# Kernel optimization log

Measured on AMD Instinct MI355X. Metric: run time of the kernel, lower is better.

## Reference

```python
import jax, jax.numpy as jnp
import numpy as np

B, N = 16, 2048
NOTE, BEAT_H, MEAS_H, FINAL_H = 512, 128, 64, 128
NUM_BEATS, NUM_MEAS = 256, 64
OUT = 11            # output_size; QPM_INDEX = 0
QPM = 0


def _uniform(k, shape, fan):
    b = 1.0 / np.sqrt(fan)
    return jax.random.uniform(k, shape, jnp.float32, -b, b)


def _lstm_cell(x, h, c, wih, whh, bih, bhh):
    g = x @ wih.T + bih + h @ whh.T + bhh
    ii, ff, gg, oo = jnp.split(g, 4, axis=-1)
    c2 = jax.nn.sigmoid(ff) * c + jax.nn.sigmoid(ii) * jnp.tanh(gg)
    return jax.nn.sigmoid(oo) * jnp.tanh(c2), c2


def setup_inputs() -> dict:
    key = jax.random.key(0)
    ks = jax.random.split(key, 20)
    note_emb = jax.random.normal(ks[0], (B, N, NOTE), jnp.float32)
    beat_emb = jax.random.normal(ks[1], (B, NUM_BEATS, BEAT_H), jnp.float32)
    measure_emb = jax.random.normal(ks[2], (B, NUM_MEAS, MEAS_H), jnp.float32)
    beat_numbers = jnp.sort(jax.random.randint(ks[3], (B, N), 0, NUM_BEATS), axis=1)
    measure_numbers = beat_numbers // (NUM_BEATS // NUM_MEAS)
    tin = BEAT_H + MEAS_H + 1 + (OUT - 1)   # beat-tempo LSTM input size
    fin = NOTE + BEAT_H + MEAS_H + OUT      # final LSTM input size
    d = OUT - 1
    return {
        "note_emb": note_emb, "beat_emb": beat_emb, "measure_emb": measure_emb,
        "beat_numbers": beat_numbers, "measure_numbers": measure_numbers,
        "Wa": _uniform(ks[4], (d, d), d), "ba": _uniform(ks[5], (d,), d),
        "ctx": _uniform(ks[6], (d,), d),
        "Wih_t": _uniform(ks[7], (4 * BEAT_H, tin), BEAT_H),
        "Whh_t": _uniform(ks[8], (4 * BEAT_H, BEAT_H), BEAT_H),
        "bih_t": _uniform(ks[9], (4 * BEAT_H,), BEAT_H),
        "bhh_t": _uniform(ks[10], (4 * BEAT_H,), BEAT_H),
        "Wih_f": _uniform(ks[11], (4 * FINAL_H, fin), FINAL_H),
        "Whh_f": _uniform(ks[12], (4 * FINAL_H, FINAL_H), FINAL_H),
        "bih_f": _uniform(ks[13], (4 * FINAL_H,), FINAL_H),
        "bhh_f": _uniform(ks[14], (4 * FINAL_H,), FINAL_H),
        "W_fc": _uniform(ks[15], (d, FINAL_H), FINAL_H),
        "b_fc": _uniform(ks[16], (d,), FINAL_H),
        "W_tfc": _uniform(ks[17], (1, BEAT_H), BEAT_H),
        "b_tfc": _uniform(ks[18], (1,), BEAT_H),
    }


def _decode(note_emb, beat_emb, measure_emb, beat_numbers, measure_numbers,
            Wa, ba, ctx, Wih_t, Whh_t, bih_t, bhh_t,
            Wih_f, Whh_f, bih_f, bhh_f, W_fc, b_fc, W_tfc, b_tfc):
    Bn, Nn = note_emb.shape[0], note_emb.shape[1]
    d = W_fc.shape[0]  # OUT - 1
    zs_beat = jnp.maximum(beat_numbers - beat_numbers[:, :1], 0)
    zs_meas = jnp.maximum(measure_numbers - measure_numbers[:, :1], 0)
    diff = jnp.diff(beat_numbers, axis=1)
    # beat_changed: first step forced to 1, then diff of beat numbers
    changed_all = jnp.concatenate([jnp.ones((Bn, 1), diff.dtype), diff], axis=1) > 0
    pos = jnp.arange(Nn)
    bidx = jnp.arange(Bn)

    carry0 = (
        jnp.zeros((Bn, BEAT_H)), jnp.zeros((Bn, BEAT_H)),        # tempo h, c
        jnp.zeros((Bn, FINAL_H)), jnp.zeros((Bn, FINAL_H)),      # final h, c
        jnp.zeros((Bn, d + 1)),                                   # prev_out
        jnp.zeros((Bn, beat_emb.shape[1], d)),                    # beat_results
        jnp.zeros((Bn, Nn, d + 1)),                               # out_total
    )

    def step(carry, i):
        th, tc, fh, fc_, prev_out, beat_results, out_total = carry
        changed = changed_all[:, i]                                # [B] bool
        # --- get_beat_corresp_out: notes j < i in the beat just finished ---
        prev_beat = beat_numbers[:, jnp.maximum(i - 1, 0)]         # [B]
        note_mask = (beat_numbers == prev_beat[:, None]) & (pos[None, :] < i)
        x = out_total[:, :, QPM + 1:]                              # [B,N,d]
        sim = (x @ Wa.T + ba) @ ctx                                # [B,N]
        sim = jnp.where(note_mask, sim, -1e9)
        w = jax.nn.softmax(sim, axis=1)
        result_node = jnp.einsum('bn,bnd->bd', w, x)
        result_node = jnp.where(note_mask.any(axis=1)[:, None], result_node, 0.0)
        cb = zs_beat[:, i]
        cm = zs_meas[:, i]
        # scatter result_node into beat_results only for batches whose beat changed
        old = beat_results[bidx, cb]
        beat_results = beat_results.at[bidx, cb].set(
            jnp.where(changed[:, None], result_node, old))
        # --- beat tempo RNN step (only applied where changed) ---
        tempo_in = jnp.concatenate([
            beat_emb[bidx, cb], measure_emb[bidx, cm],
            prev_out[:, QPM:QPM + 1], beat_results[bidx, cb]], axis=-1)
        th2, tc2 = _lstm_cell(tempo_in, th, tc, Wih_t, Whh_t, bih_t, bhh_t)
        th = jnp.where(changed[:, None], th2, th)
        tc = jnp.where(changed[:, None], tc2, tc)
        tmp_tempo = th2 @ W_tfc.T + b_tfc                          # [B,1]
        prev_out = prev_out.at[:, QPM:QPM + 1].set(
            jnp.where(changed[:, None], tmp_tempo, prev_out[:, QPM:QPM + 1]))
        # --- final note-level LSTM step (all batches) ---
        fin_in = jnp.concatenate([
            note_emb[:, i], beat_emb[bidx, cb], measure_emb[bidx, cm], prev_out], axis=-1)
        fh, fc_ = _lstm_cell(fin_in, fh, fc_, Wih_f, Whh_f, bih_f, bhh_f)
        out = fh @ W_fc.T + b_fc                                   # [B,d]
        prev_out = jnp.concatenate([prev_out[:, :QPM + 1], out], axis=-1)
        out_total = out_total.at[:, i].set(prev_out)
        return (th, tc, fh, fc_, prev_out, beat_results, out_total), None

    carry, _ = jax.lax.scan(step, carry0, jnp.arange(Nn))
    out_total = carry[-1]
    # zero out padded notes (note embedding all-zero rows)
    pad = (note_emb.sum(-1) == 0)[:, :, None]
    return jnp.where(pad, 0.0, out_total)


def reference(note_emb, beat_emb, measure_emb, beat_numbers, measure_numbers,
              Wa, ba, ctx, Wih_t, Whh_t, bih_t, bhh_t,
              Wih_f, Whh_f, bih_f, bhh_f, W_fc, b_fc, W_tfc, b_tfc):
    return _decode(note_emb, beat_emb, measure_emb, beat_numbers, measure_numbers,
                   Wa, ba, ctx, Wih_t, Whh_t, bih_t, bhh_t,
                   Wih_f, Whh_f, bih_f, bhh_f, W_fc, b_fc, W_tfc, b_tfc)
```

## Files before the change

### kernel.cpp

```cpp
#include <hip/hip_runtime.h>
#include <cstdint>
#include <cstddef>

#define B_      16
#define N_      2048
#define NOTE_   512
#define BEAT_H_ 128
#define MEAS_H_ 64
#define NBEATS_ 256
#define NMEAS_  64
#define OUT_    11
#define D_      10
#define TSTRIDE 136

typedef float f32x4 __attribute__((ext_vector_type(4)));
typedef unsigned int u32x4 __attribute__((ext_vector_type(4)));
typedef _Float16 h2v __attribute__((ext_vector_type(2)));

__device__ __forceinline__ float fexp2_(float x) {
#if __has_builtin(__builtin_amdgcn_exp2f)
    return __builtin_amdgcn_exp2f(x);
#else
    return exp2f(x);
#endif
}
__device__ __forceinline__ float frcp_(float x) {
#if __has_builtin(__builtin_amdgcn_rcpf)
    return __builtin_amdgcn_rcpf(x);
#else
    return 1.0f / x;
#endif
}
__device__ __forceinline__ float sigm_(float x) {
    return frcp_(1.0f + fexp2_(-1.4426950408889634f * x));
}
__device__ __forceinline__ float tanh_(float x) {
    return 1.0f - 2.0f * frcp_(fexp2_(2.8853900817779268f * x) + 1.0f);
}

__device__ __forceinline__ void bar_lds_() {
    asm volatile("s_waitcnt lgkmcnt(0)\n\ts_barrier" ::: "memory");
}

#define DOT4(va, vb) ((va).x * (vb).x + (va).y * (vb).y + (va).z * (vb).z + (va).w * (vb).w)

__device__ __forceinline__ float dot2f_(unsigned wu, unsigned hu, float c) {
    union { unsigned u; h2v h; } a, bb;
    a.u = wu; bb.u = hu;
#if __has_builtin(__builtin_amdgcn_fdot2)
    return __builtin_amdgcn_fdot2(a.h, bb.h, c, false);
#else
    return c + (float)a.h[0] * (float)bb.h[0] + (float)a.h[1] * (float)bb.h[1];
#endif
}

__device__ __align__(16) _Float16 g_whh_h16[512 * 128];
__device__ float g_bias_eff[512];
__device__ float g_wtail0[512];
__device__ __align__(16) _Float16 g_wht_h16[512 * TSTRIDE];

__global__ __launch_bounds__(256) void pad_k(const float* __restrict__ note,
                                             int* __restrict__ padf) {
    int wave = threadIdx.x >> 6, lane = threadIdx.x & 63;
    int r = blockIdx.x * 4 + wave;
    const float* row = note + ((size_t)r << 9);
    float s = 0.f;
#pragma unroll
    for (int u = 0; u < 8; ++u) s += row[lane + (u << 6)];
#pragma unroll
    for (int off = 32; off; off >>= 1) s += __shfl_xor(s, off, 64);
    if (lane == 0) padf[r] = (s == 0.0f) ? 1 : 0;
}

__global__ __launch_bounds__(128) void fold_whh(
    const float* __restrict__ Whh_f, const float* __restrict__ Wih_f,
    const float* __restrict__ W_fc, const float* __restrict__ b_fc) {
    int gr = blockIdx.x;
    int t = threadIdx.x;
    __shared__ float tail[OUT_];
    if (t < OUT_) tail[t] = Wih_f[(size_t)gr * 715 + 704 + t];
    __syncthreads();
    float m = Whh_f[(size_t)gr * 128 + t];
#pragma unroll
    for (int d = 0; d < D_; ++d) m += tail[1 + d] * W_fc[d * 128 + t];
    g_whh_h16[(size_t)gr * 128 + t] = (_Float16)m;
    if (t == 0) {
        float bb = 0.f;
#pragma unroll
        for (int d = 0; d < D_; ++d) bb += tail[1 + d] * b_fc[d];
        g_bias_eff[gr] = bb;
        g_wtail0[gr] = tail[0];
    }
}

__global__ __launch_bounds__(128) void fold_wht(const float* __restrict__ Whh_t) {
    int gr = blockIdx.x, t = threadIdx.x;
    g_wht_h16[(size_t)gr * TSTRIDE + t] = (_Float16)Whh_t[(size_t)gr * 128 + t];
    if (t < TSTRIDE - 128) g_wht_h16[(size_t)gr * TSTRIDE + 128 + t] = (_Float16)0.f;
}

__global__ __launch_bounds__(256) void tempo_pre_k(
    const float* __restrict__ beat, const float* __restrict__ meas,
    const int* __restrict__ bnum, const int* __restrict__ mnum,
    const float* __restrict__ Wih_t, const float* __restrict__ bih_t,
    const float* __restrict__ bhh_t, float* __restrict__ tpre) {
    __shared__ float sin_[16][192];
    int b = blockIdx.x, qt = blockIdx.y;
    int t = threadIdx.x;
    int bn0 = bnum[b << 11], mn0 = mnum[b << 11];
    for (int idx = t; idx < 16 * 192; idx += 256) {
        int qq = idx / 192, kk = idx - qq * 192;
        int q = qt * 16 + qq;
        float v;
        if (kk < 128) {
            v = beat[(size_t)(b * NBEATS_ + q) * 128 + kk];
        } else {
            int cm = ((q + bn0) >> 2) - mn0;
            if (cm > 63) cm = 63;
            if (cm < 0) cm = 0;
            v = meas[(size_t)(b * NMEAS_ + cm) * 64 + (kk - 128)];
        }
        sin_[qq][kk] = v;
    }
    __syncthreads();
    for (int half = 0; half < 2; ++half) {
        int j = t + half * 256;
        const float* wr = Wih_t + (size_t)j * 203;
        float bias = bih_t[j] + bhh_t[j];
        float acc[16] = {};
        for (int k = 0; k < 192; ++k) {
            float w = wr[k];
#pragma unroll
            for (int qq = 0; qq < 16; ++qq) acc[qq] += w * sin_[qq][k];
        }
        for (int qq = 0; qq < 16; ++qq)
            tpre[(size_t)(b * NBEATS_ + qt * 16 + qq) * 512 + j] = acc[qq] + bias;
    }
}

__global__ __launch_bounds__(256) void fin_pre_gemm(
    const float* __restrict__ note, const float* __restrict__ beat,
    const float* __restrict__ meas, const int* __restrict__ bnum,
    const int* __restrict__ mnum, const float* __restrict__ Wih_f,
    const float* __restrict__ bih_f, const float* __restrict__ bhh_f,
    float* __restrict__ finp) {
    __shared__ float As[16][64];
    __shared__ float Bs[16][64];
    int t = threadIdx.x;
    int r0 = blockIdx.x * 64;
    int j0 = blockIdx.y * 64;

    int am = t >> 2, alane = t & 3;
    int r = r0 + am;
    int b = r >> 11;
    int rb = b << 11;
    int cb = bnum[r] - bnum[rb];
    int cm = mnum[r] - mnum[rb];
    const float* arow_note = note + ((size_t)r << 9);
    const float* arow_beat = beat + ((size_t)(b * NBEATS_ + cb) << 7);
    const float* arow_meas = meas + ((size_t)(b * NMEAS_ + cm) << 6);

    int jj = t >> 2, blane = t & 3;
    const float* brow = Wih_f + (size_t)(j0 + jj) * 715;

    int tm0 = (t & 15) * 4, tn0 = (t >> 4) * 4;
    float acc[4][4] = {};

    for (int k0 = 0; k0 < 704; k0 += 16) {
        int ka = k0 + alane * 4;
        float4 av;
        if (ka < 512)      av = *(const float4*)(arow_note + ka);
        else if (ka < 640) av = *(const float4*)(arow_beat + (ka - 512));
        else               av = *(const float4*)(arow_meas + (ka - 640));
        int kb = k0 + blane * 4;
        float b0 = brow[kb], b1 = brow[kb + 1], b2 = brow[kb + 2], b3 = brow[kb + 3];
        __syncthreads();
        As[alane * 4 + 0][am] = av.x;
        As[alane * 4 + 1][am] = av.y;
        As[alane * 4 + 2][am] = av.z;
        As[alane * 4 + 3][am] = av.w;
        Bs[blane * 4 + 0][jj] = b0;
        Bs[blane * 4 + 1][jj] = b1;
        Bs[blane * 4 + 2][jj] = b2;
        Bs[blane * 4 + 3][jj] = b3;
        __syncthreads();
#pragma unroll
        for (int kk = 0; kk < 16; ++kk) {
            float4 a4 = *(const float4*)&As[kk][tm0];
            float4 b4 = *(const float4*)&Bs[kk][tn0];
            float aa[4] = {a4.x, a4.y, a4.z, a4.w};
            float bb[4] = {b4.x, b4.y, b4.z, b4.w};
#pragma unroll
            for (int mi = 0; mi < 4; ++mi)
#pragma unroll
                for (int ni = 0; ni < 4; ++ni) acc[mi][ni] += aa[mi] * bb[ni];
        }
    }
    float bias[4], beff[4];
#pragma unroll
    for (int ni = 0; ni < 4; ++ni) {
        int j = j0 + tn0 + ni;
        bias[ni] = bih_f[j] + bhh_f[j];
        beff[ni] = g_bias_eff[j];
    }
#pragma unroll
    for (int mi = 0; mi < 4; ++mi) {
        int rr = r0 + tm0 + mi;
        float eb = (rr & 2047) ? 1.0f : 0.0f;
        float4 o;
        o.x = acc[mi][0] + bias[0] + eb * beff[0];
        o.y = acc[mi][1] + bias[1] + eb * beff[1];
        o.z = acc[mi][2] + bias[2] + eb * beff[2];
        o.w = acc[mi][3] + bias[3] + eb * beff[3];
        *(float4*)(finp + ((size_t)rr << 9) + j0 + tn0) = o;
    }
}

__global__ __launch_bounds__(512)
__attribute__((amdgpu_waves_per_eu(2, 2)))
void decode_seq(
    const float* __restrict__ finp, const float* __restrict__ tpre,
    const int* __restrict__ bnum, const int* __restrict__ padf,
    const float* __restrict__ Wih_t,
    const float* __restrict__ W_fc, const float* __restrict__ b_fc,
    const float* __restrict__ W_tfc, const float* __restrict__ b_tfc,
    const float* __restrict__ Wa, const float* __restrict__ ba,
    const float* __restrict__ ctx, float* __restrict__ out,
    float* __restrict__ xg) {
    __shared__ __align__(16) _Float16 wht16_s[512 * TSTRIDE];
    __shared__ __align__(16) _Float16 ht16_s[128];
    __shared__ __align__(16) _Float16 hf16_s[128];
    __shared__ __align__(16) float hf_s[128];
    __shared__ float cf_s[128];
    __shared__ float ht_s[128];
    __shared__ float ct_s[128];
    __shared__ __align__(16) float g_s[512];
    __shared__ float gt_s[512];
    __shared__ float wtail0_s[512];
    __shared__ float wfcT[128][12];
    __shared__ float wtfc_s[128];
    __shared__ float bfc_s[12];
    __shared__ float cur_res[12];
    __shared__ float v_s[12];
    __shared__ float sc_s[4];
    __shared__ unsigned long long padw_s[32];
    __shared__ unsigned short run_start_s[300];
    __shared__ short run_cb_s[300];
    __shared__ int nruns_s;

    int t = threadIdx.x, lane = t & 63, wave = t >> 6;
    int b = blockIdx.x;

    u32x4 wf0, wf1, wf2, wf3, wf4, wf5, wf6, wf7;
    u32x4 wf8, wf9, wf10, wf11, wf12, wf13, wf14, wf15;
    {
        const u32x4* wfp = (const u32x4*)(g_whh_h16 + (size_t)t * 128);
        wf0 = wfp[0];   wf1 = wfp[1];   wf2 = wfp[2];   wf3 = wfp[3];
        wf4 = wfp[4];   wf5 = wfp[5];   wf6 = wfp[6];   wf7 = wfp[7];
        wf8 = wfp[8];   wf9 = wfp[9];   wf10 = wfp[10]; wf11 = wfp[11];
        wf12 = wfp[12]; wf13 = wfp[13]; wf14 = wfp[14]; wf15 = wfp[15];
    }
    asm volatile("" : "+v"(wf0), "+v"(wf1), "+v"(wf2), "+v"(wf3),
                      "+v"(wf4), "+v"(wf5), "+v"(wf6), "+v"(wf7));
    asm volatile("" : "+v"(wf8), "+v"(wf9), "+v"(wf10), "+v"(wf11),
                      "+v"(wf12), "+v"(wf13), "+v"(wf14), "+v"(wf15));

    float wtail0_r = g_wtail0[t];
    wtail0_s[t] = wtail0_r;
    float wiht_r[OUT_];
#pragma unroll
    for (int u = 0; u < OUT_; ++u) wiht_r[u] = Wih_t[(size_t)t * 203 + 192 + u];

    {
        const uint4* src = (const uint4*)g_wht_h16;
        uint4* dst = (uint4*)wht16_s;
#pragma unroll
        for (int k = 0; k < 17; ++k) dst[t + 512 * k] = src[t + 512 * k];
    }
    for (int k = t; k < 128 * D_; k += 512) {
        int d = k >> 7, r = k & 127;
        wfcT[r][d] = W_fc[k];
    }
    if (t < 128) {
        wtfc_s[t] = W_tfc[t];
        hf_s[t] = 0.f; cf_s[t] = 0.f; ht_s[t] = 0.f; ct_s[t] = 0.f;
        ht16_s[t] = (_Float16)0.f;
        hf16_s[t] = (_Float16)0.f;
    }
    if (t < D_) {
        bfc_s[t] = b_fc[t];
        cur_res[t] = 0.f;
        float vv = 0.f;
        for (int m = 0; m < D_; ++m) vv += ctx[m] * Wa[m * D_ + t];
        v_s[t] = vv;
    }
    if (t == 10) {
        float cc = 0.f;
        for (int m = 0; m < D_; ++m) cc += ba[m] * ctx[m];
        sc_s[0] = cc;
        sc_s[1] = b_tfc[0];
        sc_s[2] = 0.f;
    }
    if (wave >= 2 && wave < 6) {
        for (int jj = 0; jj < 8; ++jj) {
            int j = (wave - 2) * 8 + jj;
            int pv = padf[(b << 11) + j * 64 + lane];
            unsigned long long m = __ballot(pv != 0);
            if (lane == 0) padw_s[j] = m;
        }
    }
    const int* bnb = bnum + (b << 11);
    int bn0 = bnb[0];
    int base = t * 4;
    int bvm = (base == 0) ? 0 : bnb[base - 1];
    int bv0 = bnb[base], bv1 = bnb[base + 1], bv2 = bnb[base + 2], bv3 = bnb[base + 3];
    if (base == 0) bvm = bv0 - 1;
    int c = (bv0 != bvm) + (bv1 != bv0) + (bv2 != bv1) + (bv3 != bv2);
    ((int*)g_s)[t] = c;
    __syncthreads();
    if (wave == 0) {
        int c8[8], s = 0;
#pragma unroll
        for (int j = 0; j < 8; ++j) { c8[j] = ((int*)g_s)[lane * 8 + j]; s += c8[j]; }
        int incl = s;
#pragma unroll
        for (int off = 1; off < 64; off <<= 1) {
            int n = __shfl_up(incl, off, 64);
            if (lane >= off) incl += n;
        }
        int run = incl - s;
#pragma unroll
        for (int j = 0; j < 8; ++j) { ((int*)gt_s)[lane * 8 + j] = run; run += c8[j]; }
        if (lane == 63) nruns_s = incl;
    }
    __syncthreads();
    {
        int O = ((int*)gt_s)[t];
        if (bv0 != bvm) { run_start_s[O] = (unsigned short)(base + 0); run_cb_s[O] = (short)(bv0 - bn0); O++; }
        if (bv1 != bv0) { run_start_s[O] = (unsigned short)(base + 1); run_cb_s[O] = (short)(bv1 - bn0); O++; }
        if (bv2 != bv1) { run_start_s[O] = (unsigned short)(base + 2); run_cb_s[O] = (short)(bv2 - bn0); O++; }
        if (bv3 != bv2) { run_start_s[O] = (unsigned short)(base + 3); run_cb_s[O] = (short)(bv3 - bn0); O++; }
    }
    __syncthreads();
    int nruns_r = nruns_s;

    const float* finrow = finp + ((size_t)b << 11) * 512;
    float* xgb = xg + ((size_t)(b << 11)) * 16;
    float gf_cur = finrow[t];
    float gf_n1 = finrow[512 + t];
    float gt_pre = tpre[(size_t)(b * NBEATS_) * 512 + t];
    int cur_run = -1, next_start = 0, run_s = 0, S_prev = 0;

    for (int i = 0; i < N_; ++i) {
        bool changed = (i == next_start);
        if (changed) {
            cur_run++;
            S_prev = run_s;
            run_s = i;
            next_start = (cur_run + 1 < nruns_r) ? (int)run_start_s[cur_run + 1] : 4096;
        }
        float gf_n2 = finrow[(size_t)(i + 2) * 512 + t];
        float prev0 = sc_s[2];

        float acc;
        {
            const u32x4* hq = (const u32x4*)hf16_s;
            float a0 = 0.f, a1 = 0.f, a2 = 0.f, a3 = 0.f;
#define MSTEP(W, K)                                            \
            { u32x4 H = hq[K];                                 \
              a0 = dot2f_(W.x, H.x, a0);                       \
              a1 = dot2f_(W.y, H.y, a1);                       \
              a2 = dot2f_(W.z, H.z, a2);                       \
              a3 = dot2f_(W.w, H.w, a3); }
            MSTEP(wf0, 0)   MSTEP(wf1, 1)   MSTEP(wf2, 2)   MSTEP(wf3, 3)
            MSTEP(wf4, 4)   MSTEP(wf5, 5)   MSTEP(wf6, 6)   MSTEP(wf7, 7)
            MSTEP(wf8, 8)   MSTEP(wf9, 9)   MSTEP(wf10, 10) MSTEP(wf11, 11)
            MSTEP(wf12, 12) MSTEP(wf13, 13) MSTEP(wf14, 14) MSTEP(wf15, 15)
#undef MSTEP
            acc = (a0 + a1) + (a2 + a3);
        }
        {
            float g = gf_cur + acc;
            if (!changed) g += wtail0_r * prev0;
            g_s[t] = g;
        }
        gf_cur = gf_n1;
        gf_n1 = gf_n2;

        if (wave == 1 && i > 0) {
            int dd = lane >> 3, rl = lane & 7;
            int d2i = 8 + dd;
            float po1 = 0.f, po2 = 0.f;
            for (int k2 = 0; k2 < 16; ++k2) {
                int r = rl + (k2 << 3);
                float hv = hf_s[r];
                po1 += hv * wfcT[r][dd];
                if (d2i < D_) po2 += hv * wfcT[r][d2i];
            }
            po1 += __shfl_xor(po1, 1); po1 += __shfl_xor(po1, 2); po1 += __shfl_xor(po1, 4);
            po2 += __shfl_xor(po2, 1); po2 += __shfl_xor(po2, 2); po2 += __shfl_xor(po2, 4);
            int pi = i - 1;
            int pd = (int)((padw_s[pi >> 6] >> (pi & 63)) & 1ULL);
            float* orow = out + (size_t)((b << 11) + pi) * OUT_;
            float* xrow = xgb + (size_t)pi * 16;
            if (rl == 0) {
                float od = po1 + bfc_s[dd];
                xrow[dd] = od;
                orow[1 + dd] = pd ? 0.f : od;
                if (d2i < D_) {
                    float od2 = po2 + bfc_s[d2i];
                    xrow[d2i] = od2;
                    orow[1 + d2i] = pd ? 0.f : od2;
                }
            }
            if (lane == 1) orow[0] = pd ? 0.f : prev0;
        }

        if (changed) {
            float acct;
            {
                const u32x4* wq = (const u32x4*)(wht16_s + (size_t)t * TSTRIDE);
                const u32x4* hq = (const u32x4*)ht16_s;
                float a0 = 0.f, a1 = 0.f, a2 = 0.f, a3 = 0.f;
#pragma unroll
                for (int k = 0; k < 16; ++k) {
                    u32x4 W = wq[k];
                    u32x4 H = hq[k];
                    a0 = dot2f_(W.x, H.x, a0);
                    a1 = dot2f_(W.y, H.y, a1);
                    a2 = dot2f_(W.z, H.z, a2);
                    a3 = dot2f_(W.w, H.w, a3);
                }
                acct = (a0 + a1) + (a2 + a3);
            }
            gt_s[t] = gt_pre + acct + wiht_r[0] * prev0;
            __syncthreads();
        } else {
            bar_lds_();
        }

        if (!changed) {
            if (wave < 2) {
                int rr = lane + (wave << 6);
                float gi = g_s[rr], gff = g_s[128 + rr], gg = g_s[256 + rr], go = g_s[384 + rr];
                float c2 = sigm_(gff) * cf_s[rr] + sigm_(gi) * tanh_(gg);
                float h2 = sigm_(go) * tanh_(c2);
                cf_s[rr] = c2;
                hf_s[rr] = h2;
                hf16_s[rr] = (_Float16)h2;
            }
        } else {
            if (wave == 0) {
                int L = i - S_prev;
                const float4* xb = (const float4*)(xgb + (size_t)S_prev * 16);
                float lmax = -1e30f;
                for (int tt = lane; tt < L; tt += 64) {
                    float4 q0 = xb[tt * 4 + 0], q1 = xb[tt * 4 + 1], q2 = xb[tt * 4 + 2];
                    float s = sc_s[0] + q0.x * v_s[0] + q0.y * v_s[1] + q0.z * v_s[2] +
                              q0.w * v_s[3] + q1.x * v_s[4] + q1.y * v_s[5] +
                              q1.z * v_s[6] + q1.w * v_s[7] + q2.x * v_s[8] + q2.y * v_s[9];
                    lmax = fmaxf(lmax, s);
                }
#pragma unroll
                for (int off = 32; off; off >>= 1)
                    lmax = fmaxf(lmax, __shfl_xor(lmax, off, 64));
                float lsum = 0.f, lacc[D_] = {};
                for (int tt = lane; tt < L; tt += 64) {
                    float4 q0 = xb[tt * 4 + 0], q1 = xb[tt * 4 + 1], q2 = xb[tt * 4 + 2];
                    float s = sc_s[0] + q0.x * v_s[0] + q0.y * v_s[1] + q0.z * v_s[2] +
                              q0.w * v_s[3] + q1.x * v_s[4] + q1.y * v_s[5] +
                              q1.z * v_s[6] + q1.w * v_s[7] + q2.x * v_s[8] + q2.y * v_s[9];
                    float w = fexp2_(1.4426950408889634f * (s - lmax));
                    lsum += w;
                    lacc[0] += w * q0.x; lacc[1] += w * q0.y; lacc[2] += w * q0.z;
                    lacc[3] += w * q0.w; lacc[4] += w * q1.x; lacc[5] += w * q1.y;
                    lacc[6] += w * q1.z; lacc[7] += w * q1.w; lacc[8] += w * q2.x;
                    lacc[9] += w * q2.y;
                }
#pragma unroll
                for (int off = 32; off; off >>= 1) {
                    lsum += __shfl_xor(lsum, off, 64);
#pragma unroll
                    for (int d = 0; d < D_; ++d) lacc[d] += __shfl_xor(lacc[d], off, 64);
                }
                if (lane == 0) {
                    if (L > 0) {
                        float inv = 1.0f / lsum;
#pragma unroll
                        for (int d = 0; d < D_; ++d) cur_res[d] = lacc[d] * inv;
                    } else {
#pragma unroll
                        for (int d = 0; d < D_; ++d) cur_res[d] = 0.f;
                    }
                }
            }
            bar_lds_();
            {
                float gv = gt_s[t];
#pragma unroll
                for (int d = 0; d < D_; ++d) gv += wiht_r[1 + d] * cur_res[d];
                gt_s[t] = gv;
            }
            bar_lds_();
            if (wave == 0) {
                float p = 0.f;
#pragma unroll
                for (int hb = 0; hb < 2; ++hb) {
                    int rr = lane + (hb << 6);
                    float gi = gt_s[rr], gff = gt_s[128 + rr], gg = gt_s[256 + rr],
                          go = gt_s[384 + rr];
                    float c2 = sigm_(gff) * ct_s[rr] + sigm_(gi) * tanh_(gg);
                    float h2 = sigm_(go) * tanh_(c2);
                    ct_s[rr] = c2;
                    ht_s[rr] = h2;
                    ht16_s[rr] = (_Float16)h2;
                    p += h2 * wtfc_s[rr];
                }
#pragma unroll
                for (int off = 32; off; off >>= 1) p += __shfl_xor(p, off, 64);
                float tnew = p + sc_s[1];
                if (lane == 0) sc_s[2] = tnew;
#pragma unroll
                for (int hb = 0; hb < 2; ++hb) {
                    int rr = lane + (hb << 6);
                    float gi = g_s[rr] + wtail0_s[rr] * tnew;
                    float gff = g_s[128 + rr] + wtail0_s[128 + rr] * tnew;
                    float gg = g_s[256 + rr] + wtail0_s[256 + rr] * tnew;
                    float go = g_s[384 + rr] + wtail0_s[384 + rr] * tnew;
                    float c2 = sigm_(gff) * cf_s[rr] + sigm_(gi) * tanh_(gg);
                    float h2 = sigm_(go) * tanh_(c2);
                    cf_s[rr] = c2;
                    hf_s[rr] = h2;
                    hf16_s[rr] = (_Float16)h2;
                }
            }
            if (cur_run + 1 < nruns_r)
                gt_pre = tpre[(size_t)(b * NBEATS_ + (int)run_cb_s[cur_run + 1]) * 512 + t];
        }
        bar_lds_();
    }

    if (wave == 1) {
        int dd = lane >> 3, rl = lane & 7;
        int d2i = 8 + dd;
        float po1 = 0.f, po2 = 0.f;
        for (int k2 = 0; k2 < 16; ++k2) {
            int r = rl + (k2 << 3);
            float hv = hf_s[r];
            po1 += hv * wfcT[r][dd];
            if (d2i < D_) po2 += hv * wfcT[r][d2i];
        }
        po1 += __shfl_xor(po1, 1); po1 += __shfl_xor(po1, 2); po1 += __shfl_xor(po1, 4);
        po2 += __shfl_xor(po2, 1); po2 += __shfl_xor(po2, 2); po2 += __shfl_xor(po2, 4);
        int pi = N_ - 1;
        int pd = (int)((padw_s[pi >> 6] >> (pi & 63)) & 1ULL);
        float* orow = out + (size_t)((b << 11) + pi) * OUT_;
        if (rl == 0) {
            orow[1 + dd] = pd ? 0.f : (po1 + bfc_s[dd]);
            if (d2i < D_) orow[1 + d2i] = pd ? 0.f : (po2 + bfc_s[d2i]);
        }
        if (lane == 1) orow[0] = pd ? 0.f : sc_s[2];
    }
}

extern "C" void kernel_launch(void* const* d_in, const int* in_sizes, int n_in,
                              void* d_out, int out_size, void* d_ws, size_t ws_size,
                              hipStream_t stream) {
    const float* note  = (const float*)d_in[0];
    const float* beat  = (const float*)d_in[1];
    const float* meas  = (const float*)d_in[2];
    const int*   bnum  = (const int*)d_in[3];
    const int*   mnum  = (const int*)d_in[4];
    const float* Wa    = (const float*)d_in[5];
    const float* ba    = (const float*)d_in[6];
    const float* ctx   = (const float*)d_in[7];
    const float* Wih_t = (const float*)d_in[8];
    const float* Whh_t = (const float*)d_in[9];
    const float* bih_t = (const float*)d_in[10];
    const float* bhh_t = (const float*)d_in[11];
    const float* Wih_f = (const float*)d_in[12];
    const float* Whh_f = (const float*)d_in[13];
    const float* bih_f = (const float*)d_in[14];
    const float* bhh_f = (const float*)d_in[15];
    const float* W_fc  = (const float*)d_in[16];
    const float* b_fc  = (const float*)d_in[17];
    const float* W_tfc = (const float*)d_in[18];
    const float* b_tfc = (const float*)d_in[19];
    float* out = (float*)d_out;

    char* ws = (char*)d_ws;
    float* finp = (float*)ws;
    float* tpre = (float*)(ws + (size_t)64 * 1024 * 1024);
    int*   padf = (int*)(ws + (size_t)72 * 1024 * 1024);
    float* xg   = (float*)(ws + (size_t)73 * 1024 * 1024);

    pad_k<<<8192, 256, 0, stream>>>(note, padf);
    fold_whh<<<512, 128, 0, stream>>>(Whh_f, Wih_f, W_fc, b_fc);
    fold_wht<<<512, 128, 0, stream>>>(Whh_t);
    tempo_pre_k<<<dim3(16, 16), 256, 0, stream>>>(beat, meas, bnum, mnum, Wih_t,
                                                  bih_t, bhh_t, tpre);
    fin_pre_gemm<<<dim3(512, 8), 256, 0, stream>>>(note, beat, meas, bnum, mnum,
                                                   Wih_f, bih_f, bhh_f, finp);
    decode_seq<<<16, 512, 0, stream>>>(finp, tpre, bnum, padf, Wih_t,
                                       W_fc, b_fc, W_tfc, b_tfc, Wa, ba, ctx,
                                       out, xg);
}
```

Before: 4.239 ms.

## Restructure decode loop so each thread computes all four gates for one hidden unit

The sequential decode kernel moves from 512 threads, one gate row each, to 384 threads. The 256 gate threads each hold four gate rows split over two K-halves, combine the halves with a cross-lane shuffle, and apply the LSTM cell in registers. This removes the g_s/gt_s LDS round trip and one barrier per step on the non-beat-change path. Double-buffered h vectors let the next step's reads proceed without a separate sync, and dedicated waves handle the output projection and attention. The cost is more register pressure (128 weight VGPRs per thread) and reloading the Wih_t tail from global memory on every beat change.

```diff
diff --git a/kernel.cpp b/kernel.cpp
--- a/kernel.cpp
+++ b/kernel.cpp
@@ -42,8 +42,6 @@
     asm volatile("s_waitcnt lgkmcnt(0)\n\ts_barrier" ::: "memory");
 }
 
-#define DOT4(va, vb) ((va).x * (vb).x + (va).y * (vb).y + (va).z * (vb).z + (va).w * (vb).w)
-
 __device__ __forceinline__ float dot2f_(unsigned wu, unsigned hu, float c) {
     union { unsigned u; h2v h; } a, bb;
     a.u = wu; bb.u = hu;
@@ -53,6 +51,11 @@
     return c + (float)a.h[0] * (float)bb.h[0] + (float)a.h[1] * (float)bb.h[1];
 #endif
 }
+#define DQ(W, H, S)                                                           \
+    do {                                                                      \
+        S = dot2f_((W).x, (H).x, S); S = dot2f_((W).y, (H).y, S);             \
+        S = dot2f_((W).z, (H).z, S); S = dot2f_((W).w, (H).w, S);             \
+    } while (0)
 
 __device__ __align__(16) _Float16 g_whh_h16[512 * 128];
 __device__ float g_bias_eff[512];
@@ -216,7 +219,7 @@
     }
 }
 
-__global__ __launch_bounds__(512)
+__global__ __launch_bounds__(384)
 __attribute__((amdgpu_waves_per_eu(2, 2)))
 void decode_seq(
     const float* __restrict__ finp, const float* __restrict__ tpre,
@@ -228,64 +231,113 @@
     const float* __restrict__ ctx, float* __restrict__ out,
     float* __restrict__ xg) {
     __shared__ __align__(16) _Float16 wht16_s[512 * TSTRIDE];
-    __shared__ __align__(16) _Float16 ht16_s[128];
-    __shared__ __align__(16) _Float16 hf16_s[128];
-    __shared__ __align__(16) float hf_s[128];
-    __shared__ float cf_s[128];
-    __shared__ float ht_s[128];
-    __shared__ float ct_s[128];
-    __shared__ __align__(16) float g_s[512];
-    __shared__ float gt_s[512];
-    __shared__ float wtail0_s[512];
+    __shared__ __align__(16) _Float16 hf16_s[2][128];
+    __shared__ __align__(16) _Float16 ht16_s[2][128];
+    __shared__ __align__(16) float hf_s[2][128];
     __shared__ float wfcT[128][12];
     __shared__ float wtfc_s[128];
     __shared__ float bfc_s[12];
     __shared__ float cur_res[12];
     __shared__ float v_s[12];
     __shared__ float sc_s[4];
+    __shared__ float tred_s[4];
     __shared__ unsigned long long padw_s[32];
     __shared__ unsigned short run_start_s[300];
     __shared__ short run_cb_s[300];
     __shared__ int nruns_s;
 
-    int t = threadIdx.x, lane = t & 63, wave = t >> 6;
+    int t = threadIdx.x, gl = t & 63, gw = t >> 6;
     int b = blockIdx.x;
-
-    u32x4 wf0, wf1, wf2, wf3, wf4, wf5, wf6, wf7;
-    u32x4 wf8, wf9, wf10, wf11, wf12, wf13, wf14, wf15;
+    bool is_gate = gw < 4;
+    int row = (gw << 5) + (gl & 31);
+    int kh = gl >> 5;
+    if (!is_gate) row = 0;
+
+    int* counts = (int*)&wfcT[0][0];
+    int* offs = counts + 512;
+    const int* bnb = bnum + (b << 11);
+    int bn0 = bnb[0];
+    for (int c = t; c < 512; c += 384) {
+        int base = c * 4;
+        int bvm = (base == 0) ? (bnb[0] - 1) : bnb[base - 1];
+        int v0 = bnb[base], v1 = bnb[base + 1], v2 = bnb[base + 2], v3 = bnb[base + 3];
+        counts[c] = (v0 != bvm) + (v1 != v0) + (v2 != v1) + (v3 != v2);
+    }
+    __syncthreads();
+    if (gw == 0) {
+        int c8[8], s = 0;
+#pragma unroll
+        for (int j = 0; j < 8; ++j) { c8[j] = counts[gl * 8 + j]; s += c8[j]; }
+        int incl = s;
+#pragma unroll
+        for (int off = 1; off < 64; off <<= 1) {
+            int n = __shfl_up(incl, off, 64);
+            if (gl >= off) incl += n;
+        }
+        int run = incl - s;
+#pragma unroll
+        for (int j = 0; j < 8; ++j) { offs[gl * 8 + j] = run; run += c8[j]; }
+        if (gl == 63) nruns_s = incl;
+    }
+    __syncthreads();
+    for (int c = t; c < 512; c += 384) {
+        int base = c * 4;
+        int bvm = (base == 0) ? (bnb[0] - 1) : bnb[base - 1];
+        int v0 = bnb[base], v1 = bnb[base + 1], v2 = bnb[base + 2], v3 = bnb[base + 3];
+        int O = offs[c];
+        if (v0 != bvm) { run_start_s[O] = (unsigned short)(base + 0); run_cb_s[O] = (short)(v0 - bn0); O++; }
+        if (v1 != v0) { run_start_s[O] = (unsigned short)(base + 1); run_cb_s[O] = (short)(v1 - bn0); O++; }
+        if (v2 != v1) { run_start_s[O] = (unsigned short)(base + 2); run_cb_s[O] = (short)(v2 - bn0); O++; }
+        if (v3 != v2) { run_start_s[O] = (unsigned short)(base + 3); run_cb_s[O] = (short)(v3 - bn0); O++; }
+    }
+    __syncthreads();
+    int nruns_r = nruns_s;
+
+    u32x4 A0, A1, A2, A3, A4, A5, A6, A7;
+    u32x4 Bw0, Bw1, Bw2, Bw3, Bw4, Bw5, Bw6, Bw7;
+    u32x4 C0, C1, C2, C3, C4, C5, C6, C7;
+    u32x4 Dw0, Dw1, Dw2, Dw3, Dw4, Dw5, Dw6, Dw7;
     {
-        const u32x4* wfp = (const u32x4*)(g_whh_h16 + (size_t)t * 128);
-        wf0 = wfp[0];   wf1 = wfp[1];   wf2 = wfp[2];   wf3 = wfp[3];
-        wf4 = wfp[4];   wf5 = wfp[5];   wf6 = wfp[6];   wf7 = wfp[7];
-        wf8 = wfp[8];   wf9 = wfp[9];   wf10 = wfp[10]; wf11 = wfp[11];
-        wf12 = wfp[12]; wf13 = wfp[13]; wf14 = wfp[14]; wf15 = wfp[15];
-    }
-    asm volatile("" : "+v"(wf0), "+v"(wf1), "+v"(wf2), "+v"(wf3),
-                      "+v"(wf4), "+v"(wf5), "+v"(wf6), "+v"(wf7));
-    asm volatile("" : "+v"(wf8), "+v"(wf9), "+v"(wf10), "+v"(wf11),
-                      "+v"(wf12), "+v"(wf13), "+v"(wf14), "+v"(wf15));
-
-    float wtail0_r = g_wtail0[t];
-    wtail0_s[t] = wtail0_r;
-    float wiht_r[OUT_];
-#pragma unroll
-    for (int u = 0; u < OUT_; ++u) wiht_r[u] = Wih_t[(size_t)t * 203 + 192 + u];
+        int rr = is_gate ? row : 0;
+        const u32x4* pa = (const u32x4*)(g_whh_h16 + ((size_t)(rr) << 7) + (kh << 6));
+        const u32x4* pb = (const u32x4*)(g_whh_h16 + ((size_t)(rr + 128) << 7) + (kh << 6));
+        const u32x4* pc = (const u32x4*)(g_whh_h16 + ((size_t)(rr + 256) << 7) + (kh << 6));
+        const u32x4* pd = (const u32x4*)(g_whh_h16 + ((size_t)(rr + 384) << 7) + (kh << 6));
+        A0 = pa[0]; A1 = pa[1]; A2 = pa[2]; A3 = pa[3];
+        A4 = pa[4]; A5 = pa[5]; A6 = pa[6]; A7 = pa[7];
+        Bw0 = pb[0]; Bw1 = pb[1]; Bw2 = pb[2]; Bw3 = pb[3];
+        Bw4 = pb[4]; Bw5 = pb[5]; Bw6 = pb[6]; Bw7 = pb[7];
+        C0 = pc[0]; C1 = pc[1]; C2 = pc[2]; C3 = pc[3];
+        C4 = pc[4]; C5 = pc[5]; C6 = pc[6]; C7 = pc[7];
+        Dw0 = pd[0]; Dw1 = pd[1]; Dw2 = pd[2]; Dw3 = pd[3];
+        Dw4 = pd[4]; Dw5 = pd[5]; Dw6 = pd[6]; Dw7 = pd[7];
+    }
+    asm volatile("" : "+v"(A0), "+v"(A1), "+v"(A2), "+v"(A3),
+                      "+v"(A4), "+v"(A5), "+v"(A6), "+v"(A7));
+    asm volatile("" : "+v"(Bw0), "+v"(Bw1), "+v"(Bw2), "+v"(Bw3),
+                      "+v"(Bw4), "+v"(Bw5), "+v"(Bw6), "+v"(Bw7));
+    asm volatile("" : "+v"(C0), "+v"(C1), "+v"(C2), "+v"(C3),
+                      "+v"(C4), "+v"(C5), "+v"(C6), "+v"(C7));
+    asm volatile("" : "+v"(Dw0), "+v"(Dw1), "+v"(Dw2), "+v"(Dw3),
+                      "+v"(Dw4), "+v"(Dw5), "+v"(Dw6), "+v"(Dw7));
+
+    float wt0a = g_wtail0[row], wt0b = g_wtail0[row + 128],
+          wt0c = g_wtail0[row + 256], wt0d = g_wtail0[row + 384];
 
     {
         const uint4* src = (const uint4*)g_wht_h16;
         uint4* dst = (uint4*)wht16_s;
-#pragma unroll
-        for (int k = 0; k < 17; ++k) dst[t + 512 * k] = src[t + 512 * k];
-    }
-    for (int k = t; k < 128 * D_; k += 512) {
+        for (int k = t; k < 512 * TSTRIDE / 8; k += 384) dst[k] = src[k];
+    }
+    for (int k = t; k < 128 * D_; k += 384) {
         int d = k >> 7, r = k & 127;
         wfcT[r][d] = W_fc[k];
     }
     if (t < 128) {
         wtfc_s[t] = W_tfc[t];
-        hf_s[t] = 0.f; cf_s[t] = 0.f; ht_s[t] = 0.f; ct_s[t] = 0.f;
-        ht16_s[t] = (_Float16)0.f;
-        hf16_s[t] = (_Float16)0.f;
+        hf16_s[0][t] = (_Float16)0.f; hf16_s[1][t] = (_Float16)0.f;
+        ht16_s[0][t] = (_Float16)0.f; ht16_s[1][t] = (_Float16)0.f;
+        hf_s[0][t] = 0.f; hf_s[1][t] = 0.f;
     }
     if (t < D_) {
         bfc_s[t] = b_fc[t];
@@ -301,54 +353,31 @@
         sc_s[1] = b_tfc[0];
         sc_s[2] = 0.f;
     }
-    if (wave >= 2 && wave < 6) {
+    if (is_gate) {
         for (int jj = 0; jj < 8; ++jj) {
-            int j = (wave - 2) * 8 + jj;
-            int pv = padf[(b << 11) + j * 64 + lane];
+            int j = gw * 8 + jj;
+            int pv = padf[(b << 11) + j * 64 + gl];
             unsigned long long m = __ballot(pv != 0);
-            if (lane == 0) padw_s[j] = m;
-        }
-    }
-    const int* bnb = bnum + (b << 11);
-    int bn0 = bnb[0];
-    int base = t * 4;
-    int bvm = (base == 0) ? 0 : bnb[base - 1];
-    int bv0 = bnb[base], bv1 = bnb[base + 1], bv2 = bnb[base + 2], bv3 = bnb[base + 3];
-    if (base == 0) bvm = bv0 - 1;
-    int c = (bv0 != bvm) + (bv1 != bv0) + (bv2 != bv1) + (bv3 != bv2);
-    ((int*)g_s)[t] = c;
+            if (gl == 0) padw_s[j] = m;
+        }
+    }
     __syncthreads();
-    if (wave == 0) {
-        int c8[8], s = 0;
-#pragma unroll
-        for (int j = 0; j < 8; ++j) { c8[j] = ((int*)g_s)[lane * 8 + j]; s += c8[j]; }
-        int incl = s;
-#pragma unroll
-        for (int off = 1; off < 64; off <<= 1) {
-            int n = __shfl_up(incl, off, 64);
-            if (lane >= off) incl += n;
-        }
-        int run = incl - s;
-#pragma unroll
-        for (int j = 0; j < 8; ++j) { ((int*)gt_s)[lane * 8 + j] = run; run += c8[j]; }
-        if (lane == 63) nruns_s = incl;
-    }
-    __syncthreads();
-    {
-        int O = ((int*)gt_s)[t];
-        if (bv0 != bvm) { run_start_s[O] = (unsigned short)(base + 0); run_cb_s[O] = (short)(bv0 - bn0); O++; }
-        if (bv1 != bv0) { run_start_s[O] = (unsigned short)(base + 1); run_cb_s[O] = (short)(bv1 - bn0); O++; }
-        if (bv2 != bv1) { run_start_s[O] = (unsigned short)(base + 2); run_cb_s[O] = (short)(bv2 - bn0); O++; }
-        if (bv3 != bv2) { run_start_s[O] = (unsigned short)(base + 3); run_cb_s[O] = (short)(bv3 - bn0); O++; }
-    }
-    __syncthreads();
-    int nruns_r = nruns_s;
 
     const float* finrow = finp + ((size_t)b << 11) * 512;
     float* xgb = xg + ((size_t)(b << 11)) * 16;
-    float gf_cur = finrow[t];
-    float gf_n1 = finrow[512 + t];
-    float gt_pre = tpre[(size_t)(b * NBEATS_) * 512 + t];
+    float fiA_c = 0, fiB_c = 0, fiC_c = 0, fiD_c = 0;
+    float fiA_1 = 0, fiB_1 = 0, fiC_1 = 0, fiD_1 = 0;
+    float gtA = 0, gtB = 0, gtC = 0, gtD = 0;
+    if (is_gate && kh == 0) {
+        fiA_c = finrow[row];       fiB_c = finrow[row + 128];
+        fiC_c = finrow[row + 256]; fiD_c = finrow[row + 384];
+        fiA_1 = finrow[512 + row];       fiB_1 = finrow[512 + row + 128];
+        fiC_1 = finrow[512 + row + 256]; fiD_1 = finrow[512 + row + 384];
+        const float* tp0 = tpre + (size_t)(b * NBEATS_) * 512;
+        gtA = tp0[row];       gtB = tp0[row + 128];
+        gtC = tp0[row + 256]; gtD = tp0[row + 384];
+    }
+    float cf_r = 0.f, ct_r = 0.f;
     int cur_run = -1, next_start = 0, run_s = 0, S_prev = 0;
 
     for (int i = 0; i < N_; ++i) {
@@ -359,41 +388,83 @@
             run_s = i;
             next_start = (cur_run + 1 < nruns_r) ? (int)run_start_s[cur_run + 1] : 4096;
         }
-        float gf_n2 = finrow[(size_t)(i + 2) * 512 + t];
+        int wb = i & 1, rb = wb ^ 1;
+        int rp = cur_run & 1;
         float prev0 = sc_s[2];
 
-        float acc;
-        {
-            const u32x4* hq = (const u32x4*)hf16_s;
-            float a0 = 0.f, a1 = 0.f, a2 = 0.f, a3 = 0.f;
-#define MSTEP(W, K)                                            \
-            { u32x4 H = hq[K];                                 \
-              a0 = dot2f_(W.x, H.x, a0);                       \
-              a1 = dot2f_(W.y, H.y, a1);                       \
-              a2 = dot2f_(W.z, H.z, a2);                       \
-              a3 = dot2f_(W.w, H.w, a3); }
-            MSTEP(wf0, 0)   MSTEP(wf1, 1)   MSTEP(wf2, 2)   MSTEP(wf3, 3)
-            MSTEP(wf4, 4)   MSTEP(wf5, 5)   MSTEP(wf6, 6)   MSTEP(wf7, 7)
-            MSTEP(wf8, 8)   MSTEP(wf9, 9)   MSTEP(wf10, 10) MSTEP(wf11, 11)
-            MSTEP(wf12, 12) MSTEP(wf13, 13) MSTEP(wf14, 14) MSTEP(wf15, 15)
-#undef MSTEP
-            acc = (a0 + a1) + (a2 + a3);
-        }
-        {
-            float g = gf_cur + acc;
-            if (!changed) g += wtail0_r * prev0;
-            g_s[t] = g;
-        }
-        gf_cur = gf_n1;
-        gf_n1 = gf_n2;
-
-        if (wave == 1 && i > 0) {
-            int dd = lane >> 3, rl = lane & 7;
+        float si = 0.f, sf = 0.f, sg = 0.f, so = 0.f;
+        float ti = 0.f, tf = 0.f, tg = 0.f, to_ = 0.f;
+        float wA[OUT_], wB[OUT_], wC[OUT_], wD[OUT_];
+        float fA2 = 0, fB2 = 0, fC2 = 0, fD2 = 0;
+
+        if (is_gate) {
+            if (kh == 0) {
+                const float* fnx = finrow + (size_t)(i + 2) * 512;
+                fA2 = fnx[row];       fB2 = fnx[row + 128];
+                fC2 = fnx[row + 256]; fD2 = fnx[row + 384];
+            }
+            {
+                const u32x4* hq = (const u32x4*)&hf16_s[rb][0] + (kh << 3);
+                u32x4 h0 = hq[0], h1 = hq[1], h2 = hq[2], h3 = hq[3];
+                u32x4 h4 = hq[4], h5 = hq[5], h6 = hq[6], h7 = hq[7];
+                DQ(A0, h0, si); DQ(A1, h1, si); DQ(A2, h2, si); DQ(A3, h3, si);
+                DQ(A4, h4, si); DQ(A5, h5, si); DQ(A6, h6, si); DQ(A7, h7, si);
+                DQ(Bw0, h0, sf); DQ(Bw1, h1, sf); DQ(Bw2, h2, sf); DQ(Bw3, h3, sf);
+                DQ(Bw4, h4, sf); DQ(Bw5, h5, sf); DQ(Bw6, h6, sf); DQ(Bw7, h7, sf);
+                DQ(C0, h0, sg); DQ(C1, h1, sg); DQ(C2, h2, sg); DQ(C3, h3, sg);
+                DQ(C4, h4, sg); DQ(C5, h5, sg); DQ(C6, h6, sg); DQ(C7, h7, sg);
+                DQ(Dw0, h0, so); DQ(Dw1, h1, so); DQ(Dw2, h2, so); DQ(Dw3, h3, so);
+                DQ(Dw4, h4, so); DQ(Dw5, h5, so); DQ(Dw6, h6, so); DQ(Dw7, h7, so);
+            }
+            if (kh == 0) {
+                si += fiA_c; sf += fiB_c; sg += fiC_c; so += fiD_c;
+                if (!changed) {
+                    si += wt0a * prev0; sf += wt0b * prev0;
+                    sg += wt0c * prev0; so += wt0d * prev0;
+                }
+            }
+            si += __shfl_xor(si, 32, 64);
+            sf += __shfl_xor(sf, 32, 64);
+            sg += __shfl_xor(sg, 32, 64);
+            so += __shfl_xor(so, 32, 64);
+            fiA_c = fiA_1; fiB_c = fiB_1; fiC_c = fiC_1; fiD_c = fiD_1;
+            fiA_1 = fA2; fiB_1 = fB2; fiC_1 = fC2; fiD_1 = fD2;
+
+            if (changed) {
+                if (kh == 0) {
+#pragma unroll
+                    for (int u = 0; u < OUT_; ++u) {
+                        wA[u] = Wih_t[(size_t)row * 203 + 192 + u];
+                        wB[u] = Wih_t[(size_t)(row + 128) * 203 + 192 + u];
+                        wC[u] = Wih_t[(size_t)(row + 256) * 203 + 192 + u];
+                        wD[u] = Wih_t[(size_t)(row + 384) * 203 + 192 + u];
+                    }
+                }
+                const u32x4* tq = (const u32x4*)&ht16_s[rp ^ 1][0] + (kh << 3);
+                u32x4 t0 = tq[0], t1 = tq[1], t2 = tq[2], t3 = tq[3];
+                u32x4 t4 = tq[4], t5 = tq[5], t6 = tq[6], t7 = tq[7];
+                const u32x4* qa = (const u32x4*)(wht16_s + (size_t)row * TSTRIDE + (kh << 6));
+                const u32x4* qb = (const u32x4*)(wht16_s + (size_t)(row + 128) * TSTRIDE + (kh << 6));
+                const u32x4* qc = (const u32x4*)(wht16_s + (size_t)(row + 256) * TSTRIDE + (kh << 6));
+                const u32x4* qd = (const u32x4*)(wht16_s + (size_t)(row + 384) * TSTRIDE + (kh << 6));
+#pragma unroll
+                for (int k = 0; k < 8; ++k) {
+                    u32x4 hh = (k == 0) ? t0 : (k == 1) ? t1 : (k == 2) ? t2 :
+                               (k == 3) ? t3 : (k == 4) ? t4 : (k == 5) ? t5 :
+                               (k == 6) ? t6 : t7;
+                    u32x4 va = qa[k], vb = qb[k], vc = qc[k], vd = qd[k];
+                    DQ(va, hh, ti); DQ(vb, hh, tf); DQ(vc, hh, tg); DQ(vd, hh, to_);
+                }
+            }
+        }
+
+        if (gw == 4 && i > 0) {
+            int dd = gl >> 3, rl = gl & 7;
             int d2i = 8 + dd;
             float po1 = 0.f, po2 = 0.f;
             for (int k2 = 0; k2 < 16; ++k2) {
                 int r = rl + (k2 << 3);
-                float hv = hf_s[r];
+                float hv = hf_s[rb][r];
                 po1 += hv * wfcT[r][dd];
                 if (d2i < D_) po2 += hv * wfcT[r][d2i];
             }
@@ -413,48 +484,26 @@
                     orow[1 + d2i] = pd ? 0.f : od2;
                 }
             }
-            if (lane == 1) orow[0] = pd ? 0.f : prev0;
-        }
-
-        if (changed) {
-            float acct;
-            {
-                const u32x4* wq = (const u32x4*)(wht16_s + (size_t)t * TSTRIDE);
-                const u32x4* hq = (const u32x4*)ht16_s;
-                float a0 = 0.f, a1 = 0.f, a2 = 0.f, a3 = 0.f;
-#pragma unroll
-                for (int k = 0; k < 16; ++k) {
-                    u32x4 W = wq[k];
-                    u32x4 H = hq[k];
-                    a0 = dot2f_(W.x, H.x, a0);
-                    a1 = dot2f_(W.y, H.y, a1);
-                    a2 = dot2f_(W.z, H.z, a2);
-                    a3 = dot2f_(W.w, H.w, a3);
-                }
-                acct = (a0 + a1) + (a2 + a3);
-            }
-            gt_s[t] = gt_pre + acct + wiht_r[0] * prev0;
+            if (gl == 1) orow[0] = pd ? 0.f : prev0;
+        }
+
+        if (!changed) {
+            if (is_gate) {
+                float c2 = sigm_(sf) * cf_r + sigm_(si) * tanh_(sg);
+                float h2 = sigm_(so) * tanh_(c2);
+                cf_r = c2;
+                if (kh == 0) {
+                    hf16_s[wb][row] = (_Float16)h2;
+                    hf_s[wb][row] = h2;
+                }
+            }
+        } else {
             __syncthreads();
-        } else {
-            bar_lds_();
-        }
-
-        if (!changed) {
-            if (wave < 2) {
-                int rr = lane + (wave << 6);
-                float gi = g_s[rr], gff = g_s[128 + rr], gg = g_s[256 + rr], go = g_s[384 + rr];
-                float c2 = sigm_(gff) * cf_s[rr] + sigm_(gi) * tanh_(gg);
-                float h2 = sigm_(go) * tanh_(c2);
-                cf_s[rr] = c2;
-                hf_s[rr] = h2;
-                hf16_s[rr] = (_Float16)h2;
-            }
-        } else {
-            if (wave == 0) {
+            if (gw == 5) {
                 int L = i - S_prev;
                 const float4* xb = (const float4*)(xgb + (size_t)S_prev * 16);
                 float lmax = -1e30f;
-                for (int tt = lane; tt < L; tt += 64) {
+                for (int tt = gl; tt < L; tt += 64) {
                     float4 q0 = xb[tt * 4 + 0], q1 = xb[tt * 4 + 1], q2 = xb[tt * 4 + 2];
                     float s = sc_s[0] + q0.x * v_s[0] + q0.y * v_s[1] + q0.z * v_s[2] +
                               q0.w * v_s[3] + q1.x * v_s[4] + q1.y * v_s[5] +
@@ -465,7 +514,7 @@
                 for (int off = 32; off; off >>= 1)
                     lmax = fmaxf(lmax, __shfl_xor(lmax, off, 64));
                 float lsum = 0.f, lacc[D_] = {};
-                for (int tt = lane; tt < L; tt += 64) {
+                for (int tt = gl; tt < L; tt += 64) {
                     float4 q0 = xb[tt * 4 + 0], q1 = xb[tt * 4 + 1], q2 = xb[tt * 4 + 2];
                     float s = sc_s[0] + q0.x * v_s[0] + q0.y * v_s[1] + q0.z * v_s[2] +
                               q0.w * v_s[3] + q1.x * v_s[4] + q1.y * v_s[5] +
@@ -483,7 +532,7 @@
 #pragma unroll
                     for (int d = 0; d < D_; ++d) lacc[d] += __shfl_xor(lacc[d], off, 64);
                 }
-                if (lane == 0) {
+                if (gl == 0) {
                     if (L > 0) {
                         float inv = 1.0f / lsum;
 #pragma unroll
@@ -495,58 +544,65 @@
                 }
             }
             bar_lds_();
+            if (is_gate) {
+                if (kh == 0) {
+                    float ta = gtA + wA[0] * prev0, tb = gtB + wB[0] * prev0;
+                    float tc = gtC + wC[0] * prev0, td = gtD + wD[0] * prev0;
+#pragma unroll
+                    for (int d = 0; d < D_; ++d) {
+                        float cr = cur_res[d];
+                        ta += wA[1 + d] * cr; tb += wB[1 + d] * cr;
+                        tc += wC[1 + d] * cr; td += wD[1 + d] * cr;
+                    }
+                    ti += ta; tf += tb; tg += tc; to_ += td;
+                }
+                ti += __shfl_xor(ti, 32, 64);
+                tf += __shfl_xor(tf, 32, 64);
+                tg += __shfl_xor(tg, 32, 64);
+                to_ += __shfl_xor(to_, 32, 64);
+                float tc2 = sigm_(tf) * ct_r + sigm_(ti) * tanh_(tg);
+                float th2 = sigm_(to_) * tanh_(tc2);
+                ct_r = tc2;
+                if (kh == 0) ht16_s[rp][row] = (_Float16)th2;
+                float p = (kh == 0) ? th2 * wtfc_s[row] : 0.f;
+#pragma unroll
+                for (int off = 32; off; off >>= 1) p += __shfl_xor(p, off, 64);
+                if (gl == 0) tred_s[gw] = p;
+            }
+            bar_lds_();
             {
-                float gv = gt_s[t];
-#pragma unroll
-                for (int d = 0; d < D_; ++d) gv += wiht_r[1 + d] * cur_res[d];
-                gt_s[t] = gv;
-            }
-            bar_lds_();
-            if (wave == 0) {
-                float p = 0.f;
-#pragma unroll
-                for (int hb = 0; hb < 2; ++hb) {
-                    int rr = lane + (hb << 6);
-                    float gi = gt_s[rr], gff = gt_s[128 + rr], gg = gt_s[256 + rr],
-                          go = gt_s[384 + rr];
-                    float c2 = sigm_(gff) * ct_s[rr] + sigm_(gi) * tanh_(gg);
-                    float h2 = sigm_(go) * tanh_(c2);
-                    ct_s[rr] = c2;
-                    ht_s[rr] = h2;
-                    ht16_s[rr] = (_Float16)h2;
-                    p += h2 * wtfc_s[rr];
-                }
-#pragma unroll
-                for (int off = 32; off; off >>= 1) p += __shfl_xor(p, off, 64);
-                float tnew = p + sc_s[1];
-                if (lane == 0) sc_s[2] = tnew;
-#pragma unroll
-                for (int hb = 0; hb < 2; ++hb) {
-                    int rr = lane + (hb << 6);
-                    float gi = g_s[rr] + wtail0_s[rr] * tnew;
-                    float gff = g_s[128 + rr] + wtail0_s[128 + rr] * tnew;
-                    float gg = g_s[256 + rr] + wtail0_s[256 + rr] * tnew;
-                    float go = g_s[384 + rr] + wtail0_s[384 + rr] * tnew;
-                    float c2 = sigm_(gff) * cf_s[rr] + sigm_(gi) * tanh_(gg);
-                    float h2 = sigm_(go) * tanh_(c2);
-                    cf_s[rr] = c2;
-                    hf_s[rr] = h2;
-                    hf16_s[rr] = (_Float16)h2;
-                }
-            }
-            if (cur_run + 1 < nruns_r)
-                gt_pre = tpre[(size_t)(b * NBEATS_ + (int)run_cb_s[cur_run + 1]) * 512 + t];
+                float tnew = tred_s[0] + tred_s[1] + tred_s[2] + tred_s[3] + sc_s[1];
+                if (t == 0) sc_s[2] = tnew;
+                if (is_gate) {
+                    si += wt0a * tnew; sf += wt0b * tnew;
+                    sg += wt0c * tnew; so += wt0d * tnew;
+                    float c2 = sigm_(sf) * cf_r + sigm_(si) * tanh_(sg);
+                    float h2 = sigm_(so) * tanh_(c2);
+                    cf_r = c2;
+                    if (kh == 0) {
+                        hf16_s[wb][row] = (_Float16)h2;
+                        hf_s[wb][row] = h2;
+                        if (cur_run + 1 < nruns_r) {
+                            const float* tp = tpre +
+                                (size_t)(b * NBEATS_ + (int)run_cb_s[cur_run + 1]) * 512;
+                            gtA = tp[row];       gtB = tp[row + 128];
+                            gtC = tp[row + 256]; gtD = tp[row + 384];
+                        }
+                    }
+                }
+            }
         }
         bar_lds_();
     }
 
-    if (wave == 1) {
-        int dd = lane >> 3, rl = lane & 7;
+    if (gw == 4) {
+        int pb = (N_ - 1) & 1;
+        int dd = gl >> 3, rl = gl & 7;
         int d2i = 8 + dd;
         float po1 = 0.f, po2 = 0.f;
         for (int k2 = 0; k2 < 16; ++k2) {
             int r = rl + (k2 << 3);
-            float hv = hf_s[r];
+            float hv = hf_s[pb][r];
             po1 += hv * wfcT[r][dd];
             if (d2i < D_) po2 += hv * wfcT[r][d2i];
         }
@@ -559,7 +615,7 @@
             orow[1 + dd] = pd ? 0.f : (po1 + bfc_s[dd]);
             if (d2i < D_) orow[1 + d2i] = pd ? 0.f : (po2 + bfc_s[d2i]);
         }
-        if (lane == 1) orow[0] = pd ? 0.f : sc_s[2];
+        if (gl == 1) orow[0] = pd ? 0.f : sc_s[2];
     }
 }
 
@@ -601,7 +657,7 @@
                                                   bih_t, bhh_t, tpre);
     fin_pre_gemm<<<dim3(512, 8), 256, 0, stream>>>(note, beat, meas, bnum, mnum,
                                                    Wih_f, bih_f, bhh_f, finp);
-    decode_seq<<<16, 512, 0, stream>>>(finp, tpre, bnum, padf, Wih_t,
+    decode_seq<<<16, 384, 0, stream>>>(finp, tpre, bnum, padf, Wih_t,
                                        W_fc, b_fc, W_tfc, b_tfc, Wa, ba, ctx,
                                        out, xg);
 }
```

Measured after the change: 4.931 ms. 16.3% more time.
